# Kernel optimization log

Measured on AMD Instinct MI355X. Metric: run time of the kernel, lower is better.

The kernel has to match this reference:

```python
import jax, jax.numpy as jnp
import numpy as np

N = 100000      # nodes
E = 1600000     # edges (avg degree 16)
F_IN = 128      # input feature dim
HID = 64        # hidden dim per head
HEADS = 3
OUT = 2
NEG_SLOPE = 0.2  # PyG GATConv default LeakyReLU slope


def setup_inputs() -> dict:
    key = jax.random.key(0)
    ks = jax.random.split(key, 10)
    s = lambda k, shape: jax.random.normal(k, shape, jnp.float32) * 0.1
    return {
        "x": jax.random.normal(ks[0], (N, F_IN), jnp.float32),
        "edge_index": jax.random.randint(ks[1], (2, E), 0, N, dtype=jnp.int32),
        "gat1_W": s(ks[2], (F_IN, HEADS * HID)),
        "gat1_att_src": s(ks[3], (HEADS, HID)),
        "gat1_att_dst": s(ks[4], (HEADS, HID)),
        "gat1_b": jnp.zeros((HEADS * HID,), jnp.float32),
        "fc_W": s(ks[5], (HEADS * HID, HID)),
        "fc_b": jnp.zeros((HID,), jnp.float32),
        "gat2_W": s(ks[6], (HID, HEADS * OUT)),
        "gat2_att_src": s(ks[7], (HEADS, OUT)),
        "gat2_att_dst": s(ks[8], (HEADS, OUT)),
        "gat2_b": jnp.zeros((OUT,), jnp.float32),
    }


def _gat_conv(x, ei, W, att_src, att_dst, b, concat):
    """PyG GATConv: linear -> per-edge attention logits -> softmax over incoming
    edges at each dst node -> scatter-add aggregation."""
    n = x.shape[0]
    H, C = att_src.shape
    h = (x @ W).reshape(n, H, C)                       # [N,H,C]
    a_src = jnp.einsum('nhc,hc->nh', h, att_src)       # [N,H]
    a_dst = jnp.einsum('nhc,hc->nh', h, att_dst)       # [N,H]
    src, dst = ei[0], ei[1]
    e = jax.nn.leaky_relu(a_src[src] + a_dst[dst], NEG_SLOPE)  # [E,H]
    # numerically stable softmax segmented by dst node
    emax = jax.lax.stop_gradient(jax.ops.segment_max(e, dst, num_segments=n))
    ex = jnp.exp(e - emax[dst])
    denom = jax.ops.segment_sum(ex, dst, num_segments=n)
    alpha = ex / denom[dst]                            # [E,H]
    msg = h[src] * alpha[:, :, None]                   # [E,H,C] edge gather
    out = jax.ops.segment_sum(msg, dst, num_segments=n)  # [N,H,C] scatter-add
    out = out.reshape(n, H * C) if concat else out.mean(axis=1)
    return out + b


def reference(x, edge_index, gat1_W, gat1_att_src, gat1_att_dst, gat1_b,
              fc_W, fc_b, gat2_W, gat2_att_src, gat2_att_dst, gat2_b):
    # PyG GATConv add_self_loops=True
    loops = jnp.arange(x.shape[0], dtype=edge_index.dtype)
    ei = jnp.concatenate([edge_index, jnp.stack([loops, loops])], axis=1)
    h = _gat_conv(x, ei, gat1_W, gat1_att_src, gat1_att_dst, gat1_b, concat=True)
    h = jax.nn.relu(h @ fc_W + fc_b)                   # fc + relu (dropout=eval identity)
    out = _gat_conv(h, ei, gat2_W, gat2_att_src, gat2_att_dst, gat2_b, concat=False)
    return jax.nn.softmax(out, axis=1)
```

## Files before the change

kernel.cpp:

```cpp
#include <hip/hip_runtime.h>
#include <cstdint>
#include <cstddef>

typedef unsigned short ushort_t;
typedef unsigned short ushort8 __attribute__((ext_vector_type(8)));

#define LRELU(x) ((x) > 0.f ? (x) : 0.2f*(x))

__device__ __forceinline__ float bf2f(ushort_t u) {
  return __uint_as_float(((unsigned int)u) << 16);
}
__device__ __forceinline__ ushort_t f2bf(float f) {
  unsigned int b = __float_as_uint(f);
  b += 0x7fffu + ((b >> 16) & 1u);
  return (ushort_t)(b >> 16);
}
__device__ __forceinline__ float readlane_f(float v, int l) {
  return __uint_as_float(__builtin_amdgcn_readlane(__float_as_uint(v), l));
}

__device__ __forceinline__ float wave_reduce(float v) {
  #pragma unroll
  for (int m = 32; m > 0; m >>= 1) v += __shfl_xor(v, m, 64);
  return v;
}

template<bool BF16OUT, bool ATT, bool RELU, bool BIAS>
__global__ __launch_bounds__(256) void gemm256(const float* __restrict__ A,
    const float* __restrict__ Bm, const float* __restrict__ bias,
    void* __restrict__ Cout, float* __restrict__ a_s, float* __restrict__ a_d,
    const float* __restrict__ atts, const float* __restrict__ attd,
    int M, int N, int K) {
  __shared__ float As[32][260];
  __shared__ float Bs[32][68];
  const int tid = threadIdx.x;
  const int tx = tid & 7;
  const int ty = tid >> 3;
  const int r0 = blockIdx.x * 256;
  const int c0 = blockIdx.y * 64;
  float acc[8][8] = {};
  for (int k0 = 0; k0 < K; k0 += 32) {
    #pragma unroll
    for (int i = 0; i < 8; i++) {
      int f = tid + i * 256;
      int row = f >> 3, k4 = (f & 7) << 2;
      float4 v = make_float4(0.f, 0.f, 0.f, 0.f);
      int gr = r0 + row;
      if (gr < M) v = *(const float4*)(A + (size_t)gr * K + k0 + k4);
      As[k4 + 0][row] = v.x; As[k4 + 1][row] = v.y;
      As[k4 + 2][row] = v.z; As[k4 + 3][row] = v.w;
    }
    #pragma unroll
    for (int i = 0; i < 2; i++) {
      int f = tid + i * 256;
      int kr = f >> 4, c4 = (f & 15) << 2;
      *(float4*)&Bs[kr][c4] = *(const float4*)(Bm + (size_t)(k0 + kr) * N + c0 + c4);
    }
    __syncthreads();
    #pragma unroll
    for (int kk = 0; kk < 32; kk++) {
      float a[8], b[8];
      *(float4*)&a[0] = *(const float4*)&As[kk][ty * 8];
      *(float4*)&a[4] = *(const float4*)&As[kk][ty * 8 + 4];
      *(float4*)&b[0] = *(const float4*)&Bs[kk][tx * 8];
      *(float4*)&b[4] = *(const float4*)&Bs[kk][tx * 8 + 4];
      #pragma unroll
      for (int i = 0; i < 8; i++)
        #pragma unroll
        for (int j = 0; j < 8; j++)
          acc[i][j] = fmaf(a[i], b[j], acc[i][j]);
    }
    __syncthreads();
  }
  float vs[8], vd[8], bb[8];
  if (ATT) {
    #pragma unroll
    for (int j = 0; j < 8; j++) {
      vs[j] = atts[c0 + tx * 8 + j];
      vd[j] = attd[c0 + tx * 8 + j];
    }
  }
  if (BIAS) {
    #pragma unroll
    for (int j = 0; j < 8; j++) bb[j] = bias[c0 + tx * 8 + j];
  }
  #pragma unroll
  for (int i = 0; i < 8; i++) {
    int r = r0 + ty * 8 + i;
    bool ok = r < M;
    if (ATT) {
      float ps = 0.f, pd = 0.f;
      #pragma unroll
      for (int j = 0; j < 8; j++) {
        ps = fmaf(acc[i][j], vs[j], ps);
        pd = fmaf(acc[i][j], vd[j], pd);
      }
      #pragma unroll
      for (int m = 1; m < 8; m <<= 1) {
        ps += __shfl_xor(ps, m, 64);
        pd += __shfl_xor(pd, m, 64);
      }
      if (ok && tx == 0) {
        a_s[r * 3 + blockIdx.y] = ps;
        a_d[r * 3 + blockIdx.y] = pd;
      }
    }
    if (!ok) continue;
    if (BF16OUT) {
      ushort8 u;
      #pragma unroll
      for (int j = 0; j < 8; j++) u[j] = f2bf(acc[i][j]);
      *(ushort8*)((ushort_t*)Cout + (size_t)r * N + c0 + tx * 8) = u;
    } else {
      float o[8];
      #pragma unroll
      for (int j = 0; j < 8; j++) {
        o[j] = acc[i][j];
        if (BIAS) o[j] += bb[j];
        if (RELU) o[j] = fmaxf(o[j], 0.f);
      }
      float* cp = (float*)Cout + (size_t)r * N + c0 + tx * 8;
      *(float4*)cp = make_float4(o[0], o[1], o[2], o[3]);
      *(float4*)(cp + 4) = make_float4(o[4], o[5], o[6], o[7]);
    }
  }
}

__global__ void edge_rank(const int* __restrict__ dst, int* __restrict__ deg,
                          int* __restrict__ rank, int E, int Etot) {
  int e = blockIdx.x * 256 + threadIdx.x;
  if (e >= Etot) return;
  int d = (e < E) ? dst[e] : (e - E);
  rank[e] = atomicAdd(&deg[d], 1);
}

__global__ void scan1(const int* __restrict__ deg, int* __restrict__ excl,
                      int* __restrict__ bsum, int n) {
  __shared__ int sh[256];
  int t = threadIdx.x;
  int idx = blockIdx.x * 256 + t;
  int v = (idx < n) ? deg[idx] : 0;
  sh[t] = v;
  __syncthreads();
  for (int ofs = 1; ofs < 256; ofs <<= 1) {
    int add = (t >= ofs) ? sh[t - ofs] : 0;
    __syncthreads();
    sh[t] += add;
    __syncthreads();
  }
  if (idx < n) excl[idx] = sh[t] - v;
  if (t == 255) bsum[blockIdx.x] = sh[255];
}

__global__ void scan2(const int* __restrict__ bsum, int* __restrict__ boff, int nb) {
  __shared__ int sh[512];
  int t = threadIdx.x;
  int v = (t < nb) ? bsum[t] : 0;
  sh[t] = v;
  __syncthreads();
  for (int ofs = 1; ofs < 512; ofs <<= 1) {
    int add = (t >= ofs) ? sh[t - ofs] : 0;
    __syncthreads();
    sh[t] += add;
    __syncthreads();
  }
  if (t < nb) boff[t] = sh[t] - v;
}

__global__ void scan3(const int* __restrict__ excl, const int* __restrict__ boff,
                      int* __restrict__ off, int n, int etot) {
  int idx = blockIdx.x * 256 + threadIdx.x;
  if (idx < n) off[idx] = excl[idx] + boff[blockIdx.x];
  if (idx == 0) off[n] = etot;
}

__global__ void edge_place(const int* __restrict__ src, const int* __restrict__ dst,
                           const int* __restrict__ rank, const int* __restrict__ off,
                           int* __restrict__ csr, int E, int Etot) {
  int e = blockIdx.x * 256 + threadIdx.x;
  if (e >= Etot) return;
  int s, d;
  if (e < E) { s = src[e]; d = dst[e]; } else { s = d = e - E; }
  csr[off[d] + rank[e]] = s;
}

__global__ __launch_bounds__(256) void agg1_kernel(const ushort_t* __restrict__ h1,
    const float* __restrict__ a1s, const float* __restrict__ a1d,
    const int* __restrict__ off, const int* __restrict__ csr,
    const float* __restrict__ b1, float* __restrict__ out, int n) {
  int wid = (blockIdx.x * 256 + threadIdx.x) >> 6;
  int lane = threadIdx.x & 63;
  if (wid >= n) return;
  float ad0 = a1d[wid * 3 + 0], ad1 = a1d[wid * 3 + 1], ad2 = a1d[wid * 3 + 2];
  int start = off[wid], end = off[wid + 1];
  float acc0 = 0.f, acc1 = 0.f, acc2 = 0.f;
  float den0 = 0.f, den1 = 0.f, den2 = 0.f;
  for (int base = start; base < end; base += 64) {
    int cnt = min(end - base, 64);
    int sv = 0;
    float px0 = 0.f, px1 = 0.f, px2 = 0.f;
    if (lane < cnt) {
      sv = csr[base + lane];
      px0 = __expf(LRELU(a1s[sv * 3 + 0] + ad0));
      px1 = __expf(LRELU(a1s[sv * 3 + 1] + ad1));
      px2 = __expf(LRELU(a1s[sv * 3 + 2] + ad2));
      den0 += px0; den1 += px1; den2 += px2;
    }
    int j = 0;
    for (; j + 1 < cnt; j += 2) {
      int sA = __builtin_amdgcn_readlane(sv, j);
      int sB = __builtin_amdgcn_readlane(sv, j + 1);
      float xA0 = readlane_f(px0, j), xA1 = readlane_f(px1, j), xA2 = readlane_f(px2, j);
      float xB0 = readlane_f(px0, j+1), xB1 = readlane_f(px1, j+1), xB2 = readlane_f(px2, j+1);
      const ushort_t* hA = h1 + (size_t)sA * 192;
      const ushort_t* hB = h1 + (size_t)sB * 192;
      float a0 = bf2f(hA[lane]), a1v = bf2f(hA[64 + lane]), a2v = bf2f(hA[128 + lane]);
      float b0 = bf2f(hB[lane]), b1v = bf2f(hB[64 + lane]), b2v = bf2f(hB[128 + lane]);
      acc0 = fmaf(xA0, a0, acc0); acc1 = fmaf(xA1, a1v, acc1); acc2 = fmaf(xA2, a2v, acc2);
      acc0 = fmaf(xB0, b0, acc0); acc1 = fmaf(xB1, b1v, acc1); acc2 = fmaf(xB2, b2v, acc2);
    }
    if (j < cnt) {
      int sA = __builtin_amdgcn_readlane(sv, j);
      float xA0 = readlane_f(px0, j), xA1 = readlane_f(px1, j), xA2 = readlane_f(px2, j);
      const ushort_t* hA = h1 + (size_t)sA * 192;
      acc0 = fmaf(xA0, bf2f(hA[lane]),       acc0);
      acc1 = fmaf(xA1, bf2f(hA[64 + lane]),  acc1);
      acc2 = fmaf(xA2, bf2f(hA[128 + lane]), acc2);
    }
  }
  den0 = wave_reduce(den0); den1 = wave_reduce(den1); den2 = wave_reduce(den2);
  size_t o = (size_t)wid * 192;
  out[o + lane]       = acc0 / den0 + b1[lane];
  out[o + 64 + lane]  = acc1 / den1 + b1[64 + lane];
  out[o + 128 + lane] = acc2 / den2 + b1[128 + lane];
}

__global__ __launch_bounds__(256) void gemm2_pack(const float* __restrict__ hfc,
    const float* __restrict__ W2, const float* __restrict__ as2,
    const float* __restrict__ ad2, float* __restrict__ pk, int n) {
  int wid = (blockIdx.x * 256 + threadIdx.x) >> 6;
  int lane = threadIdx.x & 63;
  if (wid >= n) return;
  float hv = hfc[(size_t)wid * 64 + lane];
  float o[6];
  #pragma unroll
  for (int j = 0; j < 6; j++) o[j] = wave_reduce(hv * W2[lane * 6 + j]);
  if (lane == 0) {
    float* pp = pk + (size_t)wid * 12;
    *(float4*)pp = make_float4(o[0], o[1], o[2], o[3]);
    *(float4*)(pp + 4) = make_float4(o[4], o[5],
        o[0]*as2[0] + o[1]*as2[1], o[2]*as2[2] + o[3]*as2[3]);
    *(float4*)(pp + 8) = make_float4(o[4]*as2[4] + o[5]*as2[5],
        o[0]*ad2[0] + o[1]*ad2[1], o[2]*ad2[2] + o[3]*ad2[3],
        o[4]*ad2[4] + o[5]*ad2[5]);
  }
}

__global__ __launch_bounds__(256) void agg2_kernel(const float* __restrict__ pk,
    const int* __restrict__ off, const int* __restrict__ csr,
    const float* __restrict__ b2, float* __restrict__ outp, int n) {
  int wave = (blockIdx.x * 256 + threadIdx.x) >> 6;
  int lane = threadIdx.x & 63;
  int g = lane >> 3, sub = lane & 7;
  int d = wave * 8 + g;
  bool valid = d < n;
  float ad0 = 0.f, ad1 = 0.f, ad2v = 0.f;
  int start = 0, end = 0;
  if (valid) {
    const float* pd = pk + (size_t)d * 12;
    ad0 = pd[9]; ad1 = pd[10]; ad2v = pd[11];
    start = off[d]; end = off[d + 1];
  }
  float den0 = 0.f, den1 = 0.f, den2 = 0.f;
  float a00 = 0.f, a01 = 0.f, a10 = 0.f, a11 = 0.f, a20 = 0.f, a21 = 0.f;
  for (int j = start + sub; j < end; j += 8) {
    int s = csr[j];
    const float* ps = pk + (size_t)s * 12;
    float4 A = *(const float4*)ps;
    float4 B = *(const float4*)(ps + 4);
    float  c = ps[8];
    float x0 = __expf(LRELU(B.z + ad0));
    float x1 = __expf(LRELU(B.w + ad1));
    float x2 = __expf(LRELU(c   + ad2v));
    den0 += x0; den1 += x1; den2 += x2;
    a00 = fmaf(x0, A.x, a00); a01 = fmaf(x0, A.y, a01);
    a10 = fmaf(x1, A.z, a10); a11 = fmaf(x1, A.w, a11);
    a20 = fmaf(x2, B.x, a20); a21 = fmaf(x2, B.y, a21);
  }
  #pragma unroll
  for (int m = 1; m < 8; m <<= 1) {
    den0 += __shfl_xor(den0, m, 64); den1 += __shfl_xor(den1, m, 64);
    den2 += __shfl_xor(den2, m, 64);
    a00 += __shfl_xor(a00, m, 64); a01 += __shfl_xor(a01, m, 64);
    a10 += __shfl_xor(a10, m, 64); a11 += __shfl_xor(a11, m, 64);
    a20 += __shfl_xor(a20, m, 64); a21 += __shfl_xor(a21, m, 64);
  }
  if (valid && sub == 0) {
    float l0 = (a00/den0 + a10/den1 + a20/den2) * (1.f/3.f) + b2[0];
    float l1 = (a01/den0 + a11/den1 + a21/den2) * (1.f/3.f) + b2[1];
    float m = fmaxf(l0, l1);
    float e0 = __expf(l0 - m), e1 = __expf(l1 - m);
    float inv = 1.f / (e0 + e1);
    *(float2*)(outp + (size_t)d * 2) = make_float2(e0 * inv, e1 * inv);
  }
}

extern "C" void kernel_launch(void* const* d_in, const int* in_sizes, int n_in,
                              void* d_out, int out_size, void* d_ws, size_t ws_size,
                              hipStream_t stream) {
  const float* x   = (const float*)d_in[0];
  const int*   ei  = (const int*)d_in[1];
  const float* W1  = (const float*)d_in[2];
  const float* as1 = (const float*)d_in[3];
  const float* ad1 = (const float*)d_in[4];
  const float* b1  = (const float*)d_in[5];
  const float* fcW = (const float*)d_in[6];
  const float* fcb = (const float*)d_in[7];
  const float* W2  = (const float*)d_in[8];
  const float* as2 = (const float*)d_in[9];
  const float* ad2 = (const float*)d_in[10];
  const float* b2  = (const float*)d_in[11];
  float* outp = (float*)d_out;

  const int Nn   = in_sizes[0] / 128;
  const int E    = in_sizes[1] / 2;
  const int Etot = E + Nn;
  const int* esrc = ei;
  const int* edst = ei + E;

  char* p = (char*)d_ws;
  auto alloc = [&](size_t bytes) {
    char* q = p; p += (bytes + 255) & ~(size_t)255; return q;
  };
  ushort_t* h1bf = (ushort_t*)alloc((size_t)Nn * 192 * 2);
  float* out1  = (float*)alloc((size_t)Nn * 192 * 4);
  float* a1s   = (float*)alloc((size_t)Nn * 3 * 4);
  float* a1d   = (float*)alloc((size_t)Nn * 3 * 4);
  int* deg     = (int*)alloc((size_t)Nn * 4);
  int* off     = (int*)alloc((size_t)(Nn + 1) * 4);
  int* texcl   = (int*)alloc((size_t)Nn * 4);
  int* bsum    = (int*)alloc(512 * 4);
  int* boff    = (int*)alloc(512 * 4);
  int* csr     = (int*)alloc((size_t)Etot * 4);
  int* rank    = (int*)alloc((size_t)Etot * 4);
  float* hfc = (float*)h1bf;
  float* pk  = out1;

  hipMemsetAsync(deg, 0, (size_t)Nn * 4, stream);

  const int mb = (Nn + 255) / 256;
  const int nb4 = (Nn + 3) / 4;
  const int eb = (Etot + 255) / 256;
  const int sb = (Nn + 255) / 256;

  gemm256<true, true, false, false><<<dim3(mb, 3), 256, 0, stream>>>(
      x, W1, nullptr, h1bf, a1s, a1d, as1, ad1, Nn, 192, 128);

  edge_rank<<<eb, 256, 0, stream>>>(edst, deg, rank, E, Etot);
  scan1<<<sb, 256, 0, stream>>>(deg, texcl, bsum, Nn);
  scan2<<<1, 512, 0, stream>>>(bsum, boff, sb);
  scan3<<<sb, 256, 0, stream>>>(texcl, boff, off, Nn, Etot);
  edge_place<<<eb, 256, 0, stream>>>(esrc, edst, rank, off, csr, E, Etot);

  agg1_kernel<<<nb4, 256, 0, stream>>>(h1bf, a1s, a1d, off, csr, b1, out1, Nn);

  gemm256<false, false, true, true><<<dim3(mb, 1), 256, 0, stream>>>(
      out1, fcW, fcb, hfc, nullptr, nullptr, nullptr, nullptr, Nn, 64, 192);

  gemm2_pack<<<nb4, 256, 0, stream>>>(hfc, W2, as2, ad2, pk, Nn);

  agg2_kernel<<<(Nn + 31) / 32, 256, 0, stream>>>(pk, off, csr, b2, outp, Nn);
}
```

Baseline: 535.6 us.

## Fuse edge ranking into GEMM1, fuse layer-2 projection into FC GEMM, vectorize agg1 gathers

The edge degree/rank atomics now run as extra blocks of the first GEMM launch, so they overlap with the GEMM and one launch goes away. The FC GEMM epilogue computes the 6-wide layer-2 projection and attention terms per row from the freshly written output, which replaces the separate gemm2_pack kernel. That needs its own pk buffer, since pk previously aliased out1, which the FC GEMM reads. agg1 changes from three 2-byte loads per lane to one 8-byte load of 4 bf16 values on 48 lanes, which cuts gather instructions but leaves 16 lanes idle.

```diff
diff --git a/kernel.cpp b/kernel.cpp
--- a/kernel.cpp
+++ b/kernel.cpp
@@ -9,6 +9,12 @@
 
 __device__ __forceinline__ float bf2f(ushort_t u) {
   return __uint_as_float(((unsigned int)u) << 16);
+}
+__device__ __forceinline__ float bflo(unsigned int u) {
+  return __uint_as_float(u << 16);
+}
+__device__ __forceinline__ float bfhi(unsigned int u) {
+  return __uint_as_float(u & 0xffff0000u);
 }
 __device__ __forceinline__ ushort_t f2bf(float f) {
   unsigned int b = __float_as_uint(f);
@@ -25,19 +31,36 @@
   return v;
 }
 
-template<bool BF16OUT, bool ATT, bool RELU, bool BIAS>
+template<bool BF16OUT, bool ATT, bool RELU, bool BIAS, bool EDGE, bool PACK>
 __global__ __launch_bounds__(256) void gemm256(const float* __restrict__ A,
     const float* __restrict__ Bm, const float* __restrict__ bias,
     void* __restrict__ Cout, float* __restrict__ a_s, float* __restrict__ a_d,
     const float* __restrict__ atts, const float* __restrict__ attd,
-    int M, int N, int K) {
+    int M, int N, int K, int mb,
+    const int* __restrict__ edst, int* __restrict__ deg, int* __restrict__ rank,
+    int E, int Etot,
+    const float* __restrict__ W2, const float* __restrict__ as2,
+    const float* __restrict__ ad2, float* __restrict__ pk) {
   __shared__ float As[32][260];
   __shared__ float Bs[32][68];
   const int tid = threadIdx.x;
+  int bx, by;
+  if (EDGE) {
+    int bid = blockIdx.x;
+    if (bid >= 3 * mb) {
+      int e = (bid - 3 * mb) * 256 + tid;
+      if (e < Etot) {
+        int d = (e < E) ? edst[e] : (e - E);
+        rank[e] = atomicAdd(&deg[d], 1);
+      }
+      return;
+    }
+    bx = bid % mb; by = bid / mb;
+  } else { bx = blockIdx.x; by = blockIdx.y; }
   const int tx = tid & 7;
   const int ty = tid >> 3;
-  const int r0 = blockIdx.x * 256;
-  const int c0 = blockIdx.y * 64;
+  const int r0 = bx * 256;
+  const int c0 = by * 64;
   float acc[8][8] = {};
   for (int k0 = 0; k0 < K; k0 += 32) {
     #pragma unroll
@@ -101,8 +124,8 @@
         pd += __shfl_xor(pd, m, 64);
       }
       if (ok && tx == 0) {
-        a_s[r * 3 + blockIdx.y] = ps;
-        a_d[r * 3 + blockIdx.y] = pd;
+        a_s[r * 3 + by] = ps;
+        a_d[r * 3 + by] = pd;
       }
     }
     if (!ok) continue;
@@ -124,14 +147,31 @@
       *(float4*)(cp + 4) = make_float4(o[4], o[5], o[6], o[7]);
     }
   }
-}
-
-__global__ void edge_rank(const int* __restrict__ dst, int* __restrict__ deg,
-                          int* __restrict__ rank, int E, int Etot) {
-  int e = blockIdx.x * 256 + threadIdx.x;
-  if (e >= Etot) return;
-  int d = (e < E) ? dst[e] : (e - E);
-  rank[e] = atomicAdd(&deg[d], 1);
+  if (PACK) {
+    __syncthreads();
+    int r = r0 + tid;
+    if (r < M) {
+      const float* hp = (const float*)Cout + (size_t)r * 64;
+      float o[6] = {};
+      #pragma unroll
+      for (int k = 0; k < 64; k += 4) {
+        float4 hv = *(const float4*)(hp + k);
+        float h4[4] = {hv.x, hv.y, hv.z, hv.w};
+        #pragma unroll
+        for (int c = 0; c < 4; c++)
+          #pragma unroll
+          for (int j = 0; j < 6; j++)
+            o[j] = fmaf(h4[c], W2[(k + c) * 6 + j], o[j]);
+      }
+      float* pp = pk + (size_t)r * 12;
+      *(float4*)pp = make_float4(o[0], o[1], o[2], o[3]);
+      *(float4*)(pp + 4) = make_float4(o[4], o[5],
+          o[0]*as2[0] + o[1]*as2[1], o[2]*as2[2] + o[3]*as2[3]);
+      *(float4*)(pp + 8) = make_float4(o[4]*as2[4] + o[5]*as2[5],
+          o[0]*ad2[0] + o[1]*ad2[1], o[2]*ad2[2] + o[3]*ad2[3],
+          o[4]*ad2[4] + o[5]*ad2[5]);
+    }
+  }
 }
 
 __global__ void scan1(const int* __restrict__ deg, int* __restrict__ excl,
@@ -193,7 +233,9 @@
   if (wid >= n) return;
   float ad0 = a1d[wid * 3 + 0], ad1 = a1d[wid * 3 + 1], ad2 = a1d[wid * 3 + 2];
   int start = off[wid], end = off[wid + 1];
-  float acc0 = 0.f, acc1 = 0.f, acc2 = 0.f;
+  const int co = (lane < 48 ? lane : 47) << 2;
+  const bool s0 = lane < 16, s1 = lane < 32;
+  float acc0 = 0.f, acc1 = 0.f, acc2 = 0.f, acc3 = 0.f;
   float den0 = 0.f, den1 = 0.f, den2 = 0.f;
   for (int base = start; base < end; base += 64) {
     int cnt = min(end - base, 64);
@@ -210,49 +252,39 @@
     for (; j + 1 < cnt; j += 2) {
       int sA = __builtin_amdgcn_readlane(sv, j);
       int sB = __builtin_amdgcn_readlane(sv, j + 1);
-      float xA0 = readlane_f(px0, j), xA1 = readlane_f(px1, j), xA2 = readlane_f(px2, j);
-      float xB0 = readlane_f(px0, j+1), xB1 = readlane_f(px1, j+1), xB2 = readlane_f(px2, j+1);
-      const ushort_t* hA = h1 + (size_t)sA * 192;
-      const ushort_t* hB = h1 + (size_t)sB * 192;
-      float a0 = bf2f(hA[lane]), a1v = bf2f(hA[64 + lane]), a2v = bf2f(hA[128 + lane]);
-      float b0 = bf2f(hB[lane]), b1v = bf2f(hB[64 + lane]), b2v = bf2f(hB[128 + lane]);
-      acc0 = fmaf(xA0, a0, acc0); acc1 = fmaf(xA1, a1v, acc1); acc2 = fmaf(xA2, a2v, acc2);
-      acc0 = fmaf(xB0, b0, acc0); acc1 = fmaf(xB1, b1v, acc1); acc2 = fmaf(xB2, b2v, acc2);
+      float a0 = readlane_f(px0, j), a1v = readlane_f(px1, j), a2v = readlane_f(px2, j);
+      float b0 = readlane_f(px0, j+1), b1v = readlane_f(px1, j+1), b2v = readlane_f(px2, j+1);
+      float xA = s0 ? a0 : (s1 ? a1v : a2v);
+      float xB = s0 ? b0 : (s1 ? b1v : b2v);
+      uint2 uA = *(const uint2*)(h1 + (size_t)sA * 192 + co);
+      uint2 uB = *(const uint2*)(h1 + (size_t)sB * 192 + co);
+      acc0 = fmaf(xA, bflo(uA.x), acc0);
+      acc1 = fmaf(xA, bfhi(uA.x), acc1);
+      acc2 = fmaf(xA, bflo(uA.y), acc2);
+      acc3 = fmaf(xA, bfhi(uA.y), acc3);
+      acc0 = fmaf(xB, bflo(uB.x), acc0);
+      acc1 = fmaf(xB, bfhi(uB.x), acc1);
+      acc2 = fmaf(xB, bflo(uB.y), acc2);
+      acc3 = fmaf(xB, bfhi(uB.y), acc3);
     }
     if (j < cnt) {
       int sA = __builtin_amdgcn_readlane(sv, j);
-      float xA0 = readlane_f(px0, j), xA1 = readlane_f(px1, j), xA2 = readlane_f(px2, j);
-      const ushort_t* hA = h1 + (size_t)sA * 192;
-      acc0 = fmaf(xA0, bf2f(hA[lane]),       acc0);
-      acc1 = fmaf(xA1, bf2f(hA[64 + lane]),  acc1);
-      acc2 = fmaf(xA2, bf2f(hA[128 + lane]), acc2);
+      float a0 = readlane_f(px0, j), a1v = readlane_f(px1, j), a2v = readlane_f(px2, j);
+      float xA = s0 ? a0 : (s1 ? a1v : a2v);
+      uint2 uA = *(const uint2*)(h1 + (size_t)sA * 192 + co);
+      acc0 = fmaf(xA, bflo(uA.x), acc0);
+      acc1 = fmaf(xA, bfhi(uA.x), acc1);
+      acc2 = fmaf(xA, bflo(uA.y), acc2);
+      acc3 = fmaf(xA, bfhi(uA.y), acc3);
     }
   }
   den0 = wave_reduce(den0); den1 = wave_reduce(den1); den2 = wave_reduce(den2);
-  size_t o = (size_t)wid * 192;
-  out[o + lane]       = acc0 / den0 + b1[lane];
-  out[o + 64 + lane]  = acc1 / den1 + b1[64 + lane];
-  out[o + 128 + lane] = acc2 / den2 + b1[128 + lane];
-}
-
-__global__ __launch_bounds__(256) void gemm2_pack(const float* __restrict__ hfc,
-    const float* __restrict__ W2, const float* __restrict__ as2,
-    const float* __restrict__ ad2, float* __restrict__ pk, int n) {
-  int wid = (blockIdx.x * 256 + threadIdx.x) >> 6;
-  int lane = threadIdx.x & 63;
-  if (wid >= n) return;
-  float hv = hfc[(size_t)wid * 64 + lane];
-  float o[6];
-  #pragma unroll
-  for (int j = 0; j < 6; j++) o[j] = wave_reduce(hv * W2[lane * 6 + j]);
-  if (lane == 0) {
-    float* pp = pk + (size_t)wid * 12;
-    *(float4*)pp = make_float4(o[0], o[1], o[2], o[3]);
-    *(float4*)(pp + 4) = make_float4(o[4], o[5],
-        o[0]*as2[0] + o[1]*as2[1], o[2]*as2[2] + o[3]*as2[3]);
-    *(float4*)(pp + 8) = make_float4(o[4]*as2[4] + o[5]*as2[5],
-        o[0]*ad2[0] + o[1]*ad2[1], o[2]*ad2[2] + o[3]*ad2[3],
-        o[4]*ad2[4] + o[5]*ad2[5]);
+  if (lane < 48) {
+    float den = s0 ? den0 : (s1 ? den1 : den2);
+    float4 bb = *(const float4*)(b1 + (lane << 2));
+    float* op = out + (size_t)wid * 192 + (lane << 2);
+    *(float4*)op = make_float4(acc0 / den + bb.x, acc1 / den + bb.y,
+                               acc2 / den + bb.z, acc3 / den + bb.w);
   }
 }
 
@@ -334,6 +366,7 @@
   };
   ushort_t* h1bf = (ushort_t*)alloc((size_t)Nn * 192 * 2);
   float* out1  = (float*)alloc((size_t)Nn * 192 * 4);
+  float* pk    = (float*)alloc((size_t)Nn * 12 * 4);
   float* a1s   = (float*)alloc((size_t)Nn * 3 * 4);
   float* a1d   = (float*)alloc((size_t)Nn * 3 * 4);
   int* deg     = (int*)alloc((size_t)Nn * 4);
@@ -344,7 +377,6 @@
   int* csr     = (int*)alloc((size_t)Etot * 4);
   int* rank    = (int*)alloc((size_t)Etot * 4);
   float* hfc = (float*)h1bf;
-  float* pk  = out1;
 
   hipMemsetAsync(deg, 0, (size_t)Nn * 4, stream);
 
@@ -353,10 +385,10 @@
   const int eb = (Etot + 255) / 256;
   const int sb = (Nn + 255) / 256;
 
-  gemm256<true, true, false, false><<<dim3(mb, 3), 256, 0, stream>>>(
-      x, W1, nullptr, h1bf, a1s, a1d, as1, ad1, Nn, 192, 128);
-
-  edge_rank<<<eb, 256, 0, stream>>>(edst, deg, rank, E, Etot);
+  gemm256<true, true, false, false, true, false><<<3 * mb + eb, 256, 0, stream>>>(
+      x, W1, nullptr, h1bf, a1s, a1d, as1, ad1, Nn, 192, 128, mb,
+      edst, deg, rank, E, Etot, nullptr, nullptr, nullptr, nullptr);
+
   scan1<<<sb, 256, 0, stream>>>(deg, texcl, bsum, Nn);
   scan2<<<1, 512, 0, stream>>>(bsum, boff, sb);
   scan3<<<sb, 256, 0, stream>>>(texcl, boff, off, Nn, Etot);
@@ -364,10 +396,9 @@
 
   agg1_kernel<<<nb4, 256, 0, stream>>>(h1bf, a1s, a1d, off, csr, b1, out1, Nn);
 
-  gemm256<false, false, true, true><<<dim3(mb, 1), 256, 0, stream>>>(
-      out1, fcW, fcb, hfc, nullptr, nullptr, nullptr, nullptr, Nn, 64, 192);
-
-  gemm2_pack<<<nb4, 256, 0, stream>>>(hfc, W2, as2, ad2, pk, Nn);
+  gemm256<false, false, true, true, false, true><<<mb, 256, 0, stream>>>(
+      out1, fcW, fcb, hfc, nullptr, nullptr, nullptr, nullptr, Nn, 64, 192, mb,
+      nullptr, nullptr, nullptr, 0, 0, W2, as2, ad2, pk);
 
   agg2_kernel<<<(Nn + 31) / 32, 256, 0, stream>>>(pk, off, csr, b2, outp, Nn);
 }
```

Measured after the change: 490.3 us. 8.5% less time.
